# Optimization experiments

Measured on AMD Instinct MI355X. Metric: run time of the kernel, lower is better.

The kernel has to match this reference:

```python
import jax, jax.numpy as jnp
import numpy as np

N_OUT, N_CONS, N_AGE = 7, 20, 15
H = 256
B, T = 64, 365
D_ECO = N_CONS + N_AGE          # 35: eco+age feed the shared eco LSTM
D_BR = 1 + 3 + H                # 260: init + 3 age cols + eco LSTM output


def setup_inputs() -> dict:
    key = jax.random.key(0)
    ks = jax.random.split(key, 24)
    s = 0.05
    w = lambda k, shape: (jax.random.normal(k, shape, jnp.float32) * s)
    z = lambda shape: jnp.zeros(shape, jnp.float32)
    return {
        "inputs": jax.random.normal(ks[0], (B, T, N_CONS + N_OUT + N_AGE), jnp.float32),
        # shared eco LSTM (n_lstm_eco = 1)
        "eco_Wk": w(ks[1], (D_ECO, 4 * H)), "eco_Wr": w(ks[2], (H, 4 * H)), "eco_b": z((4 * H,)),
        # per-output data LSTMs (tanh)
        "data_Wk": w(ks[3], (N_OUT, D_BR, 4 * H)), "data_Wr": w(ks[4], (N_OUT, H, 4 * H)), "data_b": z((N_OUT, 4 * H)),
        # per-output attention LSTMs (activation='sigmoid')
        "att_Wk": w(ks[5], (N_OUT, D_BR, 4 * H)), "att_Wr": w(ks[6], (N_OUT, H, 4 * H)), "att_b": z((N_OUT, 4 * H)),
        # per-output tsOut LSTMs (return last state)
        "ts_Wk": w(ks[7], (N_OUT, H, 4 * H)), "ts_Wr": w(ks[8], (N_OUT, H, 4 * H)), "ts_b": z((N_OUT, 4 * H)),
        # per-output dense heads
        "d1_W": w(ks[9], (N_OUT, H, 256)), "d1_b": z((N_OUT, 256)),
        "d2_W": w(ks[10], (N_OUT, 256, 64)), "d2_b": z((N_OUT, 64)),
        "df_W": w(ks[11], (N_OUT, 64 + 3, 1)), "df_b": z((N_OUT, 1)),
    }


def _lstm(x, Wk, Wr, b, act):
    """Keras-style LSTM. x: [B,T,D]. Returns (all hidden [B,T,H], last hidden [B,H])."""
    Bc = x.shape[0]
    Hc = Wr.shape[0]
    xW = jnp.einsum('btd,dg->btg', x, Wk) + b      # precompute input projections

    def step(carry, xt):
        h, c = carry
        zi, zf, zg, zo = jnp.split(xt + h @ Wr, 4, axis=-1)  # Keras gate order i,f,c,o
        c = jax.nn.sigmoid(zf) * c + jax.nn.sigmoid(zi) * act(zg)
        h = jax.nn.sigmoid(zo) * act(c)
        return (h, c), h

    init = (jnp.zeros((Bc, Hc), x.dtype), jnp.zeros((Bc, Hc), x.dtype))
    (hT, _), hs = jax.lax.scan(step, init, jnp.swapaxes(xW, 0, 1))
    return jnp.swapaxes(hs, 0, 1), hT


def _branch(init_i, age_i, dWk, dWr, db, aWk, aWr, ab, tWk, tWr, tb, w1, b1, w2, b2, wf, bf, x_ecos):
    # init_i: [B,T,1], age_i: [B,T,3], x_ecos: [B,T,H] (shared)
    cur_input = jnp.concatenate([init_i, age_i, x_ecos], axis=-1)  # [B,T,260]
    data_hs, _ = _lstm(cur_input, dWk, dWr, db, jnp.tanh)
    att_hs, _ = _lstm(cur_input, aWk, aWr, ab, jax.nn.sigmoid)     # activation='sigmoid'
    _, h_last = _lstm(data_hs * att_hs, tWk, tWr, tb, jnp.tanh)    # return_sequences=False
    h = jax.nn.relu(h_last @ w1 + b1)
    h = jax.nn.relu(h @ w2 + b2)
    h = jnp.concatenate([h, cur_input[:, -1, 1:4]], axis=-1)       # append last-step age cols
    out = h @ wf + bf + cur_input[:, -1, :1]                       # residual add of last init
    return out  # [B,1]


def reference(inputs, eco_Wk, eco_Wr, eco_b, data_Wk, data_Wr, data_b,
              att_Wk, att_Wr, att_b, ts_Wk, ts_Wr, ts_b,
              d1_W, d1_b, d2_W, d2_b, df_W, df_b):
    x_init = inputs[:, :, N_CONS:N_CONS + N_OUT]                       # [B,T,7]
    x_age = inputs[:, :, N_CONS + N_OUT:N_CONS + N_OUT + N_AGE]        # [B,T,15]
    x_eco = inputs[:, :, :N_CONS]                                      # [B,T,20]

    x_ecos, _ = _lstm(jnp.concatenate([x_eco, x_age], axis=-1), eco_Wk, eco_Wr, eco_b, jnp.tanh)  # [B,T,256]

    init_i = jnp.moveaxis(x_init, 2, 0)[..., None]                     # [7,B,T,1]
    i_idx = jnp.arange(N_OUT)
    age_cols = jnp.stack([jnp.zeros_like(i_idx), i_idx + 1, i_idx + 8], axis=1)  # [7,3]
    age_i = jnp.moveaxis(x_age[:, :, age_cols], 2, 0)                  # [7,B,T,3]

    outs = jax.vmap(_branch, in_axes=(0,) * 17 + (None,))(
        init_i, age_i, data_Wk, data_Wr, data_b, att_Wk, att_Wr, att_b,
        ts_Wk, ts_Wr, ts_b, d1_W, d1_b, d2_W, d2_b, df_W, df_b, x_ecos)  # [7,B,1]
    return jnp.transpose(outs[:, :, 0])  # [B,7]
```

## Files before the change

### kernel.cpp

```cpp
#include <hip/hip_runtime.h>


#define TT 365
#define RE 4
#define RS 4

typedef short bf16x8 __attribute__((ext_vector_type(8)));
typedef float f32x4 __attribute__((ext_vector_type(4)));

__device__ __forceinline__ float b2f(unsigned short u) {
  union { unsigned u32; float f; } v; v.u32 = ((unsigned)u) << 16; return v.f;
}
__device__ __forceinline__ unsigned short f2b(float f) {
  union { float f; unsigned u32; } v; v.f = f;
  unsigned u = v.u32;
  u = u + 0x7FFFu + ((u >> 16) & 1u);
  return (unsigned short)(u >> 16);
}
__device__ __forceinline__ float sigf(float x) { return 1.0f / (1.0f + __expf(-x)); }
__device__ __forceinline__ float tanh_(float x) { return 2.0f / (1.0f + __expf(-2.0f * x)) - 1.0f; }

__device__ __forceinline__ unsigned long long ld64(const unsigned long long* p) {
  return __hip_atomic_load(p, __ATOMIC_RELAXED, __HIP_MEMORY_SCOPE_AGENT);
}
__device__ __forceinline__ void st64(unsigned long long* p, unsigned long long v) {
  __hip_atomic_store(p, v, __ATOMIC_RELAXED, __HIP_MEMORY_SCOPE_AGENT);
}
__device__ __forceinline__ unsigned ld32(const unsigned* p) {
  return __hip_atomic_load(p, __ATOMIC_RELAXED, __HIP_MEMORY_SCOPE_AGENT);
}
__device__ __forceinline__ void st32(unsigned* p, unsigned v) {
  __hip_atomic_store(p, v, __ATOMIC_RELAXED, __HIP_MEMORY_SCOPE_AGENT);
}
__device__ __forceinline__ unsigned long long tag2(unsigned tag, float a, float b) {
  return ((unsigned long long)tag << 32) | (unsigned)f2b(a) | ((unsigned)f2b(b) << 16);
}

__global__ __launch_bounds__(256) void k0a_wr(const float* __restrict__ eco_Wr,
    const float* __restrict__ data_Wr, const float* __restrict__ att_Wr,
    const float* __restrict__ ts_Wr, unsigned short* __restrict__ wr_swz)
{
  __shared__ float ls[32 * 133];
  const int kb = blockIdx.x, wg = blockIdx.y, l = blockIdx.z, tid = threadIdx.x;
  const float* src;
  if (l == 0) src = eco_Wr;
  else if (l < 15) { int d = l - 1; src = ((d & 1) ? att_Wr : data_Wr) + (size_t)(d >> 1) * 262144; }
  else src = ts_Wr + (size_t)(l - 15) * 262144;
  for (int e = tid; e < 4096; e += 256) {
    int ks = e >> 7, col = e & 127;
    int gate = col >> 5, hi = col & 31;
    ls[ks * 133 + col] = src[(size_t)(kb * 32 + ks) * 1024 + gate * 256 + wg * 32 + hi];
  }
  __syncthreads();
  unsigned short* out = wr_swz + (((size_t)l * 8 + wg) * 8 + kb) * 4096;
  for (int e = tid; e < 4096; e += 256) {
    int col = e >> 5, ks = e & 31;
    out[e] = f2b(ls[ks * 133 + col]);
  }
}

__global__ __launch_bounds__(256) void k0b_wk(const float* __restrict__ data_Wk,
    const float* __restrict__ att_Wk, const float* __restrict__ ts_Wk,
    unsigned short* __restrict__ wk_da, unsigned short* __restrict__ wk_ts)
{
  __shared__ float ls[32 * 261];
  const int cc = blockIdx.x, kb = blockIdx.y, d = blockIdx.z, tid = threadIdx.x;
  const float* src; unsigned short* dst; int roff;
  if (d < 14) { src = ((d & 1) ? att_Wk : data_Wk) + (size_t)(d >> 1) * 266240;
                dst = wk_da + (size_t)d * 262144; roff = 4; }
  else { src = ts_Wk + (size_t)(d - 14) * 262144;
         dst = wk_ts + (size_t)(d - 14) * 262144; roff = 0; }
  for (int e = tid; e < 8192; e += 256) {
    int ks = e >> 8, c2 = e & 255;
    ls[ks * 261 + c2] = src[(size_t)(roff + kb * 32 + ks) * 1024 + cc * 256 + c2];
  }
  __syncthreads();
  for (int e = tid; e < 8192; e += 256) {
    int col2 = e >> 5, ks = e & 31;
    dst[(size_t)kb * 32768 + (cc * 256 + col2) * 32 + ks] = f2b(ls[ks * 261 + col2]);
  }
}

__global__ __launch_bounds__(256) void k1_ecoxw(const float* __restrict__ inputs,
    const float* __restrict__ eco_Wk, const float* __restrict__ eco_b,
    unsigned short* __restrict__ xw_eco)
{
  __shared__ float Asl[64 * 35];
  __shared__ float Bsl[35 * 256];
  const int tg = blockIdx.x, ct = blockIdx.y, tid = threadIdx.x;
  for (int i = tid; i < 64 * 35; i += 256) {
    int b = i / 35, k = i - b * 35;
    int col = (k < 20) ? k : (k + 7);
    Asl[i] = inputs[((size_t)b * TT + tg) * 42 + col];
  }
  for (int i = tid; i < 35 * 256; i += 256) {
    int k = i >> 8, c = i & 255;
    Bsl[i] = eco_Wk[(size_t)k * 1024 + ct * 256 + c];
  }
  __syncthreads();
  const float bias = eco_b[ct * 256 + tid];
  for (int r = 0; r < 64; ++r) {
    float s = bias;
    #pragma unroll
    for (int k = 0; k < 35; ++k) s += Asl[r * 35 + k] * Bsl[k * 256 + tid];
    xw_eco[((size_t)tg * 64 + r) * 1024 + ct * 256 + tid] = f2b(s);
  }
}

__global__ __launch_bounds__(256, 1) void kP(
    const unsigned short* __restrict__ wr_swz,
    const unsigned short* __restrict__ wk_da,
    const unsigned short* __restrict__ wk_ts,
    const unsigned short* __restrict__ xw_eco,
    const float* __restrict__ inputs,
    const float* __restrict__ data_Wk, const float* __restrict__ att_Wk,
    const float* __restrict__ data_b, const float* __restrict__ att_b,
    const float* __restrict__ ts_b,
    unsigned long long* __restrict__ hE,
    unsigned long long* __restrict__ hD,
    unsigned long long* __restrict__ hsD,
    unsigned long long* __restrict__ hsA,
    unsigned long long* __restrict__ h2,
    unsigned* __restrict__ hDf, unsigned* __restrict__ h2f,
    unsigned* __restrict__ roleCtr,
    float* __restrict__ h_last)
{
  __shared__ __align__(16) unsigned char smem[160256];
  __shared__ int role_s;
  const int tid = threadIdx.x;
  if (tid == 0) {
    unsigned xcc;
    asm volatile("s_getreg_b32 %0, hwreg(HW_REG_XCC_ID)" : "=s"(xcc));
    xcc &= 7u;
    unsigned slot = atomicAdd(&roleCtr[xcc], 1u);
    role_s = (int)(xcc * 256u + slot);
  }
  __syncthreads();
  const int xcd = role_s >> 8, slot = role_s & 255;
  if (slot >= 32) return;
  const int lane = tid & 63, w = tid >> 6, c = lane & 15, grp = lane >> 4;

  if (xcd == 7) {
    if (slot >= 16) return;
    unsigned short* WR = (unsigned short*)smem;
    unsigned short* Hs = (unsigned short*)(smem + 81920);
    float* zsh = (float*)(smem + 102400);
    float* cst = (float*)(smem + 119296);
    const int wg = slot >> 1, bg = slot & 1;
    const unsigned short* wr_g = wr_swz + (size_t)wg * 32768;
    for (int i = tid * 8; i < 32768; i += 2048) {
      int kb = i >> 12; int rr = i & 4095; int col = rr >> 5; int ks = rr & 31;
      *(uint4*)&WR[(kb * 128 + col) * 40 + ks] = *(const uint4*)&wr_g[i];
    }
    for (int i = tid; i < 1024; i += 256) cst[i] = 0.0f;

    int xoff[16];
    #pragma unroll
    for (int rt = 0; rt < 2; ++rt)
      #pragma unroll
      for (int ct = 0; ct < 2; ++ct)
        #pragma unroll
        for (int rg = 0; rg < 4; ++rg)
          xoff[(rt * 2 + ct) * 4 + rg] =
              (bg * 32 + rt * 16 + grp * 4 + rg) * 1024 + w * 256 + wg * 32 + ct * 16 + c;
    unsigned short xv[16], xn[16];
    #pragma unroll
    for (int i = 0; i < 16; ++i) xv[i] = xw_eco[xoff[i]];
    __syncthreads();

    for (int t = 0; t < TT; ++t) {
      if (t + 1 > RE && tid < 112) {
        while ((int)ld32(&hDf[tid]) < t + 1 - RE) __builtin_amdgcn_s_sleep(2);
      }
      {
        const unsigned long long* hb = hE + (size_t)(t % RE) * 8192;
        unsigned long long v[16];
        #pragma unroll
        for (int i = 0; i < 16; ++i) {
          int m = tid + i * 256;
          v[i] = ld64(&hb[(bg * 32 + (m >> 7)) * 128 + (m & 127)]);
        }
        const unsigned tagv = (unsigned)t;
        int tries = 0;
        while (true) {
          unsigned pend = 0u;
          #pragma unroll
          for (int i = 0; i < 16; ++i)
            pend |= ((unsigned)(v[i] >> 32) != tagv) ? (1u << i) : 0u;
          if (!pend) break;
          if (++tries > 8) __builtin_amdgcn_s_sleep(1);
          #pragma unroll
          for (int i = 0; i < 16; ++i)
            if (pend & (1u << i)) {
              int m = tid + i * 256;
              v[i] = ld64(&hb[(bg * 32 + (m >> 7)) * 128 + (m & 127)]);
            }
        }
        #pragma unroll
        for (int i = 0; i < 16; ++i) {
          int m = tid + i * 256, row = m >> 7, kp = m & 127;
          *(unsigned int*)&Hs[((kp >> 4) * 32 + row) * 40 + 2 * (kp & 15)] = (unsigned int)v[i];
        }
      }
      __syncthreads();
      f32x4 acc[4];
      #pragma unroll
      for (int i = 0; i < 4; ++i)
        #pragma unroll
        for (int rg = 0; rg < 4; ++rg) acc[i][rg] = b2f(xv[i * 4 + rg]);
      if (t + 1 < TT) {
        const unsigned short* xw1 = xw_eco + (size_t)(t + 1) * 65536;
        #pragma unroll
        for (int i = 0; i < 16; ++i) xn[i] = xw1[xoff[i]];
      }
      #pragma unroll
      for (int kb = 0; kb < 8; ++kb) {
        bf16x8 a0 = *(const bf16x8*)&Hs[(kb * 32 + c) * 40 + grp * 8];
        bf16x8 a1 = *(const bf16x8*)&Hs[(kb * 32 + 16 + c) * 40 + grp * 8];
        bf16x8 b0 = *(const bf16x8*)&WR[(kb * 128 + w * 32 + c) * 40 + grp * 8];
        bf16x8 b1 = *(const bf16x8*)&WR[(kb * 128 + w * 32 + 16 + c) * 40 + grp * 8];
        acc[0] = __builtin_amdgcn_mfma_f32_16x16x32_bf16(a0, b0, acc[0], 0, 0, 0);
        acc[1] = __builtin_amdgcn_mfma_f32_16x16x32_bf16(a0, b1, acc[1], 0, 0, 0);
        acc[2] = __builtin_amdgcn_mfma_f32_16x16x32_bf16(a1, b0, acc[2], 0, 0, 0);
        acc[3] = __builtin_amdgcn_mfma_f32_16x16x32_bf16(a1, b1, acc[3], 0, 0, 0);
      }
      #pragma unroll
      for (int i = 0; i < 4; ++i) {
        int rt = i >> 1, ct = i & 1;
        #pragma unroll
        for (int rg = 0; rg < 4; ++rg)
          zsh[(rt * 16 + grp * 4 + rg) * 132 + w * 32 + ct * 16 + c] = acc[i][rg];
      }
      __syncthreads();
      {
        int row = tid >> 3, hq8 = tid & 7;
        float4 zi = *(const float4*)&zsh[row * 132 +      hq8 * 4];
        float4 zf = *(const float4*)&zsh[row * 132 + 32 + hq8 * 4];
        float4 zg = *(const float4*)&zsh[row * 132 + 64 + hq8 * 4];
        float4 zo = *(const float4*)&zsh[row * 132 + 96 + hq8 * 4];
        float4 c0 = *(const float4*)&cst[row * 32 + hq8 * 4];
        float cn0 = sigf(zf.x) * c0.x + sigf(zi.x) * tanh_(zg.x);
        float cn1 = sigf(zf.y) * c0.y + sigf(zi.y) * tanh_(zg.y);
        float cn2 = sigf(zf.z) * c0.z + sigf(zi.z) * tanh_(zg.z);
        float cn3 = sigf(zf.w) * c0.w + sigf(zi.w) * tanh_(zg.w);
        float hv0 = sigf(zo.x) * tanh_(cn0);
        float hv1 = sigf(zo.y) * tanh_(cn1);
        float hv2 = sigf(zo.z) * tanh_(cn2);
        float hv3 = sigf(zo.w) * tanh_(cn3);
        *(float4*)&cst[row * 32 + hq8 * 4] = make_float4(cn0, cn1, cn2, cn3);
        unsigned long long* ho = hE + (size_t)((t + 1) % RE) * 8192
                               + (bg * 32 + row) * 128 + wg * 16 + hq8 * 2;
        st64(&ho[0], tag2(t + 1, hv0, hv1));
        st64(&ho[1], tag2(t + 1, hv2, hv3));
      }
      #pragma unroll
      for (int i = 0; i < 16; ++i) xv[i] = xn[i];
    }
  } else if (slot < 16) {
    unsigned short* WR = (unsigned short*)smem;
    unsigned short* Hs = (unsigned short*)(smem + 81920);
    float* zsh = (float*)(smem + 122880);
    float* a_sp = (float*)(smem + 156672);
    float* b_sp = (float*)(smem + 157696);
    float* bias_s = (float*)(smem + 159744);
    const int l1 = xcd * 2 + (slot >> 3), colwg = slot & 7, br = xcd;
    const int q = l1 * 8 + colwg;
    const bool act_sig = (l1 & 1);
    const unsigned short* wr_g = wr_swz + ((size_t)(1 + l1) * 8 + colwg) * 32768;
    for (int i = tid * 8; i < 32768; i += 2048) {
      int kb = i >> 12; int rr = i & 4095; int col = rr >> 5; int ks = rr & 31;
      *(uint4*)&WR[(kb * 128 + col) * 40 + ks] = *(const uint4*)&wr_g[i];
    }
    bf16x8 wkf[16];
    const unsigned short* wk = wk_da + (size_t)l1 * 262144;
    #pragma unroll
    for (int kb = 0; kb < 8; ++kb)
      #pragma unroll
      for (int ct = 0; ct < 2; ++ct) {
        int col = w * 256 + colwg * 32 + ct * 16 + c;
        wkf[kb * 2 + ct] = *(const bf16x8*)&wk[kb * 32768 + col * 32 + grp * 8];
      }
    const float* spWk = (act_sig ? att_Wk : data_Wk) + (size_t)br * 266240;
    for (int i = tid; i < 512; i += 256) {
      int j = i >> 7, colL = i & 127;
      int gcol = (colL >> 5) * 256 + colwg * 32 + (colL & 31);
      b_sp[i] = spWk[(size_t)j * 1024 + gcol];
    }
    if (tid < 128) {
      int gcol = (tid >> 5) * 256 + colwg * 32 + (tid & 31);
      bias_s[tid] = (act_sig ? att_b : data_b)[br * 1024 + gcol];
    }
    float creg[8];
    #pragma unroll
    for (int j = 0; j < 8; ++j) creg[j] = 0.0f;
    unsigned long long* hDl = hD + (size_t)l1 * 2 * 8192;
    unsigned long long* ring = (act_sig ? hsA : hsD) + (size_t)br * RS * 8192;
    __syncthreads();

    for (int t = 0; t < TT; ++t) {
      if (t + 1 > RS && tid < 16) {
        while ((int)ld32(&h2f[br * 16 + tid]) < t + 1 - RS) __builtin_amdgcn_s_sleep(2);
      }
      if (tid < 64) {
        const float* ip = inputs + ((size_t)tid * TT + t) * 42;
        a_sp[tid * 4 + 0] = ip[20 + br];
        a_sp[tid * 4 + 1] = ip[27];
        a_sp[tid * 4 + 2] = ip[27 + br + 1];
        a_sp[tid * 4 + 3] = ip[27 + br + 8];
      }
      const unsigned long long* he = hE + (size_t)((t + 1) % RE) * 8192;
      const unsigned long long* ho = hDl + (size_t)(t & 1) * 8192;
      unsigned long long ve[32], vh[32];
      #pragma unroll
      for (int i = 0; i < 32; ++i) ve[i] = ld64(&he[tid + i * 256]);
      #pragma unroll
      for (int i = 0; i < 32; ++i) vh[i] = ld64(&ho[tid + i * 256]);
      {
        const unsigned tagv = (unsigned)(t + 1);
        int tries = 0;
        while (true) {
          unsigned long long pend = 0ull;
          #pragma unroll
          for (int i = 0; i < 32; ++i)
            pend |= ((unsigned)(ve[i] >> 32) != tagv) ? (1ull << i) : 0ull;
          if (!pend) break;
          if (++tries > 8) __builtin_amdgcn_s_sleep(1);
          #pragma unroll
          for (int i = 0; i < 32; ++i)
            if (pend & (1ull << i)) ve[i] = ld64(&he[tid + i * 256]);
        }
      }
      #pragma unroll
      for (int i = 0; i < 32; ++i) {
        int m = tid + i * 256, row = m >> 7, kp = m & 127;
        *(unsigned int*)&Hs[((kp >> 4) * 64 + row) * 40 + 2 * (kp & 15)] = (unsigned int)ve[i];
      }
      __syncthreads();
      if (tid == 0) st32(&hDf[q], (unsigned)(t + 1));
      f32x4 acc[8] = {};
      #pragma unroll
      for (int kb = 0; kb < 8; ++kb) {
        bf16x8 a[4];
        #pragma unroll
        for (int rt = 0; rt < 4; ++rt)
          a[rt] = *(const bf16x8*)&Hs[(kb * 64 + rt * 16 + c) * 40 + grp * 8];
        #pragma unroll
        for (int rt = 0; rt < 4; ++rt)
          #pragma unroll
          for (int ct = 0; ct < 2; ++ct)
            acc[rt * 2 + ct] = __builtin_amdgcn_mfma_f32_16x16x32_bf16(a[rt], wkf[kb * 2 + ct], acc[rt * 2 + ct], 0, 0, 0);
      }
      #pragma unroll
      for (int i = 0; i < 8; ++i) {
        int rt = i >> 1, ct2 = i & 1;
        #pragma unroll
        for (int rg = 0; rg < 4; ++rg) {
          int row = rt * 16 + grp * 4 + rg;
          int colL = w * 32 + ct2 * 16 + c;
          acc[i][rg] += bias_s[colL]
                      + a_sp[row * 4 + 0] * b_sp[colL]       + a_sp[row * 4 + 1] * b_sp[128 + colL]
                      + a_sp[row * 4 + 2] * b_sp[256 + colL] + a_sp[row * 4 + 3] * b_sp[384 + colL];
        }
      }
      {
        const unsigned tagv = (unsigned)t;
        int tries = 0;
        while (true) {
          unsigned long long pend = 0ull;
          #pragma unroll
          for (int i = 0; i < 32; ++i)
            pend |= ((unsigned)(vh[i] >> 32) != tagv) ? (1ull << i) : 0ull;
          if (!pend) break;
          if (++tries > 8) __builtin_amdgcn_s_sleep(1);
          #pragma unroll
          for (int i = 0; i < 32; ++i)
            if (pend & (1ull << i)) vh[i] = ld64(&ho[tid + i * 256]);
        }
      }
      __syncthreads();
      #pragma unroll
      for (int i = 0; i < 32; ++i) {
        int m = tid + i * 256, row = m >> 7, kp = m & 127;
        *(unsigned int*)&Hs[((kp >> 4) * 64 + row) * 40 + 2 * (kp & 15)] = (unsigned int)vh[i];
      }
      __syncthreads();
      #pragma unroll
      for (int kb = 0; kb < 8; ++kb) {
        bf16x8 a[4]; bf16x8 b[2];
        #pragma unroll
        for (int rt = 0; rt < 4; ++rt)
          a[rt] = *(const bf16x8*)&Hs[(kb * 64 + rt * 16 + c) * 40 + grp * 8];
        #pragma unroll
        for (int ct = 0; ct < 2; ++ct)
          b[ct] = *(const bf16x8*)&WR[(kb * 128 + w * 32 + ct * 16 + c) * 40 + grp * 8];
        #pragma unroll
        for (int rt = 0; rt < 4; ++rt)
          #pragma unroll
          for (int ct = 0; ct < 2; ++ct)
            acc[rt * 2 + ct] = __builtin_amdgcn_mfma_f32_16x16x32_bf16(a[rt], b[ct], acc[rt * 2 + ct], 0, 0, 0);
      }
      #pragma unroll
      for (int i = 0; i < 8; ++i) {
        int rt = i >> 1, ct2 = i & 1;
        #pragma unroll
        for (int rg = 0; rg < 4; ++rg)
          zsh[(rt * 16 + grp * 4 + rg) * 132 + w * 32 + ct2 * 16 + c] = acc[i][rg];
      }
      __syncthreads();
      {
        unsigned long long* hon = hDl + (size_t)((t + 1) & 1) * 8192;
        unsigned long long* rs = ring + (size_t)(t % RS) * 8192;
        #pragma unroll
        for (int it = 0; it < 2; ++it) {
          int m = tid + it * 256, row = m >> 3, hq8 = m & 7;
          float4 zi = *(const float4*)&zsh[row * 132 +      hq8 * 4];
          float4 zf = *(const float4*)&zsh[row * 132 + 32 + hq8 * 4];
          float4 zg = *(const float4*)&zsh[row * 132 + 64 + hq8 * 4];
          float4 zo = *(const float4*)&zsh[row * 132 + 96 + hq8 * 4];
          float g0 = act_sig ? sigf(zg.x) : tanh_(zg.x);
          float g1 = act_sig ? sigf(zg.y) : tanh_(zg.y);
          float g2 = act_sig ? sigf(zg.z) : tanh_(zg.z);
          float g3 = act_sig ? sigf(zg.w) : tanh_(zg.w);
          float cn0 = sigf(zf.x) * creg[it * 4 + 0] + sigf(zi.x) * g0;
          float cn1 = sigf(zf.y) * creg[it * 4 + 1] + sigf(zi.y) * g1;
          float cn2 = sigf(zf.z) * creg[it * 4 + 2] + sigf(zi.z) * g2;
          float cn3 = sigf(zf.w) * creg[it * 4 + 3] + sigf(zi.w) * g3;
          float hv0 = sigf(zo.x) * (act_sig ? sigf(cn0) : tanh_(cn0));
          float hv1 = sigf(zo.y) * (act_sig ? sigf(cn1) : tanh_(cn1));
          float hv2 = sigf(zo.z) * (act_sig ? sigf(cn2) : tanh_(cn2));
          float hv3 = sigf(zo.w) * (act_sig ? sigf(cn3) : tanh_(cn3));
          creg[it * 4 + 0] = cn0; creg[it * 4 + 1] = cn1;
          creg[it * 4 + 2] = cn2; creg[it * 4 + 3] = cn3;
          int kp = colwg * 16 + hq8 * 2;
          unsigned long long w0 = tag2(t + 1, hv0, hv1);
          unsigned long long w1 = tag2(t + 1, hv2, hv3);
          st64(&hon[row * 128 + kp], w0);
          st64(&hon[row * 128 + kp + 1], w1);
          st64(&rs[row * 128 + kp], w0);
          st64(&rs[row * 128 + kp + 1], w1);
        }
      }
    }
  } else {
    unsigned short* WR = (unsigned short*)smem;
    unsigned short* Hs = (unsigned short*)(smem + 81920);
    float* zsh = (float*)(smem + 102400);
    float* bias_s = (float*)(smem + 119296);
    const int d = xcd, sub = slot - 16, colwg = sub >> 1, bg = sub & 1;
    const unsigned short* wr_g = wr_swz + ((size_t)(15 + d) * 8 + colwg) * 32768;
    for (int i = tid * 8; i < 32768; i += 2048) {
      int kb = i >> 12; int rr = i & 4095; int col = rr >> 5; int ks = rr & 31;
      *(uint4*)&WR[(kb * 128 + col) * 40 + ks] = *(const uint4*)&wr_g[i];
    }
    bf16x8 wkf[16];
    const unsigned short* wk = wk_ts + (size_t)d * 262144;
    #pragma unroll
    for (int kb = 0; kb < 8; ++kb)
      #pragma unroll
      for (int ct = 0; ct < 2; ++ct) {
        int col = w * 256 + colwg * 32 + ct * 16 + c;
        wkf[kb * 2 + ct] = *(const bf16x8*)&wk[kb * 32768 + col * 32 + grp * 8];
      }
    if (tid < 128) {
      int gcol = (tid >> 5) * 256 + colwg * 32 + (tid & 31);
      bias_s[tid] = ts_b[d * 1024 + gcol];
    }
    float creg[4] = {0.0f, 0.0f, 0.0f, 0.0f};
    const unsigned long long* rD = hsD + (size_t)d * RS * 8192;
    const unsigned long long* rA = hsA + (size_t)d * RS * 8192;
    unsigned long long* h2d = h2 + (size_t)d * 2 * 8192;
    __syncthreads();

    for (int t = 0; t < TT; ++t) {
      const unsigned long long* sd = rD + (size_t)(t % RS) * 8192;
      const unsigned long long* sa = rA + (size_t)(t % RS) * 8192;
      const unsigned long long* ho = h2d + (size_t)(t & 1) * 8192;
      unsigned long long vd[16], va[16], vh[16];
      int idx16[16];
      #pragma unroll
      for (int i = 0; i < 16; ++i) {
        int m = tid + i * 256;
        idx16[i] = (bg * 32 + (m >> 7)) * 128 + (m & 127);
      }
      #pragma unroll
      for (int i = 0; i < 16; ++i) vd[i] = ld64(&sd[idx16[i]]);
      #pragma unroll
      for (int i = 0; i < 16; ++i) va[i] = ld64(&sa[idx16[i]]);
      #pragma unroll
      for (int i = 0; i < 16; ++i) vh[i] = ld64(&ho[idx16[i]]);
      {
        const unsigned tagv = (unsigned)(t + 1);
        int tries = 0;
        while (true) {
          unsigned pend = 0u;
          #pragma unroll
          for (int i = 0; i < 16; ++i) {
            pend |= ((unsigned)(vd[i] >> 32) != tagv) ? (1u << i) : 0u;
            pend |= ((unsigned)(va[i] >> 32) != tagv) ? (0x10000u << i) : 0u;
          }
          if (!pend) break;
          if (++tries > 8) __builtin_amdgcn_s_sleep(1);
          #pragma unroll
          for (int i = 0; i < 16; ++i) {
            if (pend & (1u << i)) vd[i] = ld64(&sd[idx16[i]]);
            if (pend & (0x10000u << i)) va[i] = ld64(&sa[idx16[i]]);
          }
        }
      }
      #pragma unroll
      for (int i = 0; i < 16; ++i) {
        int m = tid + i * 256, row = m >> 7, kp = m & 127;
        unsigned dl = (unsigned)vd[i], al = (unsigned)va[i];
        float p0 = b2f((unsigned short)dl) * b2f((unsigned short)al);
        float p1 = b2f((unsigned short)(dl >> 16)) * b2f((unsigned short)(al >> 16));
        unsigned pv = (unsigned)f2b(p0) | ((unsigned)f2b(p1) << 16);
        *(unsigned int*)&Hs[((kp >> 4) * 32 + row) * 40 + 2 * (kp & 15)] = pv;
      }
      __syncthreads();
      if (tid == 0) st32(&h2f[d * 16 + sub], (unsigned)(t + 1));
      f32x4 acc[4] = {};
      #pragma unroll
      for (int kb = 0; kb < 8; ++kb) {
        bf16x8 a0 = *(const bf16x8*)&Hs[(kb * 32 + c) * 40 + grp * 8];
        bf16x8 a1 = *(const bf16x8*)&Hs[(kb * 32 + 16 + c) * 40 + grp * 8];
        acc[0] = __builtin_amdgcn_mfma_f32_16x16x32_bf16(a0, wkf[kb * 2 + 0], acc[0], 0, 0, 0);
        acc[1] = __builtin_amdgcn_mfma_f32_16x16x32_bf16(a0, wkf[kb * 2 + 1], acc[1], 0, 0, 0);
        acc[2] = __builtin_amdgcn_mfma_f32_16x16x32_bf16(a1, wkf[kb * 2 + 0], acc[2], 0, 0, 0);
        acc[3] = __builtin_amdgcn_mfma_f32_16x16x32_bf16(a1, wkf[kb * 2 + 1], acc[3], 0, 0, 0);
      }
      #pragma unroll
      for (int i = 0; i < 4; ++i) {
        int ct2 = i & 1;
        #pragma unroll
        for (int rg = 0; rg < 4; ++rg)
          acc[i][rg] += bias_s[w * 32 + ct2 * 16 + c];
      }
      {
        const unsigned tagv = (unsigned)t;
        int tries = 0;
        while (true) {
          unsigned pend = 0u;
          #pragma unroll
          for (int i = 0; i < 16; ++i)
            pend |= ((unsigned)(vh[i] >> 32) != tagv) ? (1u << i) : 0u;
          if (!pend) break;
          if (++tries > 8) __builtin_amdgcn_s_sleep(1);
          #pragma unroll
          for (int i = 0; i < 16; ++i)
            if (pend & (1u << i)) vh[i] = ld64(&ho[idx16[i]]);
        }
      }
      __syncthreads();
      #pragma unroll
      for (int i = 0; i < 16; ++i) {
        int m = tid + i * 256, row = m >> 7, kp = m & 127;
        *(unsigned int*)&Hs[((kp >> 4) * 32 + row) * 40 + 2 * (kp & 15)] = (unsigned int)vh[i];
      }
      __syncthreads();
      #pragma unroll
      for (int kb = 0; kb < 8; ++kb) {
        bf16x8 a0 = *(const bf16x8*)&Hs[(kb * 32 + c) * 40 + grp * 8];
        bf16x8 a1 = *(const bf16x8*)&Hs[(kb * 32 + 16 + c) * 40 + grp * 8];
        bf16x8 b0 = *(const bf16x8*)&WR[(kb * 128 + w * 32 + c) * 40 + grp * 8];
        bf16x8 b1 = *(const bf16x8*)&WR[(kb * 128 + w * 32 + 16 + c) * 40 + grp * 8];
        acc[0] = __builtin_amdgcn_mfma_f32_16x16x32_bf16(a0, b0, acc[0], 0, 0, 0);
        acc[1] = __builtin_amdgcn_mfma_f32_16x16x32_bf16(a0, b1, acc[1], 0, 0, 0);
        acc[2] = __builtin_amdgcn_mfma_f32_16x16x32_bf16(a1, b0, acc[2], 0, 0, 0);
        acc[3] = __builtin_amdgcn_mfma_f32_16x16x32_bf16(a1, b1, acc[3], 0, 0, 0);
      }
      #pragma unroll
      for (int i = 0; i < 4; ++i) {
        int rt = i >> 1, ct2 = i & 1;
        #pragma unroll
        for (int rg = 0; rg < 4; ++rg)
          zsh[(rt * 16 + grp * 4 + rg) * 132 + w * 32 + ct2 * 16 + c] = acc[i][rg];
      }
      __syncthreads();
      {
        int row = tid >> 3, hq8 = tid & 7;
        float4 zi = *(const float4*)&zsh[row * 132 +      hq8 * 4];
        float4 zf = *(const float4*)&zsh[row * 132 + 32 + hq8 * 4];
        float4 zg = *(const float4*)&zsh[row * 132 + 64 + hq8 * 4];
        float4 zo = *(const float4*)&zsh[row * 132 + 96 + hq8 * 4];
        float cn0 = sigf(zf.x) * creg[0] + sigf(zi.x) * tanh_(zg.x);
        float cn1 = sigf(zf.y) * creg[1] + sigf(zi.y) * tanh_(zg.y);
        float cn2 = sigf(zf.z) * creg[2] + sigf(zi.z) * tanh_(zg.z);
        float cn3 = sigf(zf.w) * creg[3] + sigf(zi.w) * tanh_(zg.w);
        float hv0 = sigf(zo.x) * tanh_(cn0);
        float hv1 = sigf(zo.y) * tanh_(cn1);
        float hv2 = sigf(zo.z) * tanh_(cn2);
        float hv3 = sigf(zo.w) * tanh_(cn3);
        creg[0] = cn0; creg[1] = cn1; creg[2] = cn2; creg[3] = cn3;
        unsigned long long* hn = h2d + (size_t)((t + 1) & 1) * 8192
                               + (bg * 32 + row) * 128 + colwg * 16 + hq8 * 2;
        st64(&hn[0], tag2(t + 1, hv0, hv1));
        st64(&hn[1], tag2(t + 1, hv2, hv3));
        if (t == TT - 1) {
          *(float4*)&h_last[(size_t)d * 16384 + (bg * 32 + row) * 256 + colwg * 32 + hq8 * 4]
              = make_float4(hv0, hv1, hv2, hv3);
        }
      }
    }
  }
}

__global__ __launch_bounds__(256) void k7_d1(const float* __restrict__ h_last,
    const float* __restrict__ d1_W, const float* __restrict__ d1_b, float* __restrict__ d1o)
{
  __shared__ float Asl[64 * 256];
  __shared__ float Bsl[256 * 64];
  const int nt = blockIdx.x, br = blockIdx.y, tid = threadIdx.x;
  const float* hl = h_last + (size_t)br * 16384;
  for (int i = tid; i < 16384; i += 256) Asl[i] = hl[i];
  const float* wp = d1_W + (size_t)br * 65536 + nt * 64;
  for (int i = tid; i < 16384; i += 256) {
    int k = i >> 6, cl = i & 63;
    Bsl[i] = wp[(size_t)k * 256 + cl];
  }
  __syncthreads();
  const int cl = tid & 63, rq = tid >> 6;
  float s[16];
  const float bias = d1_b[br * 256 + nt * 64 + cl];
  #pragma unroll
  for (int i = 0; i < 16; ++i) s[i] = bias;
  for (int k = 0; k < 256; ++k) {
    float bv = Bsl[k * 64 + cl];
    #pragma unroll
    for (int i = 0; i < 16; ++i) s[i] += Asl[(rq * 16 + i) * 256 + k] * bv;
  }
  #pragma unroll
  for (int i = 0; i < 16; ++i)
    d1o[(size_t)br * 16384 + (rq * 16 + i) * 256 + nt * 64 + cl] = fmaxf(s[i], 0.0f);
}

__global__ __launch_bounds__(256) void k8_head(const float* __restrict__ d1o,
    const float* __restrict__ d2_W, const float* __restrict__ d2_b,
    const float* __restrict__ df_W, const float* __restrict__ df_b,
    const float* __restrict__ inputs, float* __restrict__ out)
{
  __shared__ float Asl[64 * 256];
  __shared__ float Bsl[256 * 64];
  __shared__ float d2sT[64 * 65];
  __shared__ float wfs[68];
  const int br = blockIdx.x, tid = threadIdx.x;
  for (int i = tid; i < 16384; i += 256) Asl[i] = d1o[(size_t)br * 16384 + i];
  for (int i = tid; i < 16384; i += 256) Bsl[i] = d2_W[(size_t)br * 16384 + i];
  if (tid < 67) wfs[tid] = df_W[br * 67 + tid];
  __syncthreads();
  const int cl = tid & 63, rq = tid >> 6;
  float s[16];
  const float bias = d2_b[br * 64 + cl];
  #pragma unroll
  for (int i = 0; i < 16; ++i) s[i] = bias;
  for (int k = 0; k < 256; ++k) {
    float bv = Bsl[k * 64 + cl];
    #pragma unroll
    for (int i = 0; i < 16; ++i) s[i] += Asl[(rq * 16 + i) * 256 + k] * bv;
  }
  #pragma unroll
  for (int i = 0; i < 16; ++i) d2sT[cl * 65 + rq * 16 + i] = fmaxf(s[i], 0.0f);
  __syncthreads();
  if (tid < 64) {
    const int b = tid;
    const float* ip = inputs + ((size_t)b * TT + (TT - 1)) * 42;
    float acc = df_b[br] + ip[20 + br] + ip[27] * wfs[64] + ip[27 + br + 1] * wfs[65]
              + ip[27 + br + 8] * wfs[66];
    #pragma unroll 4
    for (int j = 0; j < 64; ++j) acc += d2sT[j * 65 + b] * wfs[j];
    out[b * 7 + br] = acc;
  }
}

extern "C" void kernel_launch(void* const* d_in, const int* in_sizes, int n_in,
                              void* d_out, int out_size, void* d_ws, size_t ws_size,
                              hipStream_t stream) {
  (void)in_sizes; (void)n_in; (void)out_size;
  const float* inputs  = (const float*)d_in[0];
  const float* eco_Wk  = (const float*)d_in[1];
  const float* eco_Wr  = (const float*)d_in[2];
  const float* eco_b   = (const float*)d_in[3];
  const float* data_Wk = (const float*)d_in[4];
  const float* data_Wr = (const float*)d_in[5];
  const float* data_b  = (const float*)d_in[6];
  const float* att_Wk  = (const float*)d_in[7];
  const float* att_Wr  = (const float*)d_in[8];
  const float* att_b   = (const float*)d_in[9];
  const float* ts_Wk   = (const float*)d_in[10];
  const float* ts_Wr   = (const float*)d_in[11];
  const float* ts_b    = (const float*)d_in[12];
  const float* d1_W    = (const float*)d_in[13];
  const float* d1_b    = (const float*)d_in[14];
  const float* d2_W    = (const float*)d_in[15];
  const float* d2_b    = (const float*)d_in[16];
  const float* df_W    = (const float*)d_in[17];
  const float* df_b    = (const float*)d_in[18];

  char* ws = (char*)d_ws;
  size_t off = 0;
  auto take = [&](size_t bytes) -> void* {
    void* p = ws + off;
    off += (bytes + 255) & ~(size_t)255;
    return p;
  };
  unsigned short* wr_swz = (unsigned short*)take((size_t)22 * 262144 * 2);
  unsigned short* wk_da  = (unsigned short*)take((size_t)14 * 262144 * 2);
  unsigned short* wk_ts  = (unsigned short*)take((size_t)7  * 262144 * 2);
  unsigned short* xw_eco = (unsigned short*)take((size_t)TT * 65536 * 2);
  float*          h_last = (float*)take((size_t)7 * 16384 * 4);
  float*          d1o    = (float*)take((size_t)7 * 16384 * 4);
  size_t sync_begin = off;
  unsigned long long* hE  = (unsigned long long*)take((size_t)RE * 8192 * 8);
  unsigned long long* hD  = (unsigned long long*)take((size_t)14 * 2 * 8192 * 8);
  unsigned long long* hsD = (unsigned long long*)take((size_t)7 * RS * 8192 * 8);
  unsigned long long* hsA = (unsigned long long*)take((size_t)7 * RS * 8192 * 8);
  unsigned long long* h2  = (unsigned long long*)take((size_t)7 * 2 * 8192 * 8);
  unsigned* hDf = (unsigned*)take(112 * 4);
  unsigned* h2f = (unsigned*)take(112 * 4);
  unsigned* roleCtr = (unsigned*)take(16 * 4);
  size_t sync_bytes = off - sync_begin;
  if (off > ws_size) return;

  hipMemsetAsync(ws + sync_begin, 0, sync_bytes, stream);
  k0a_wr<<<dim3(8, 8, 22), 256, 0, stream>>>(eco_Wr, data_Wr, att_Wr, ts_Wr, wr_swz);
  k0b_wk<<<dim3(4, 8, 21), 256, 0, stream>>>(data_Wk, att_Wk, ts_Wk, wk_da, wk_ts);
  k1_ecoxw<<<dim3(TT, 4), 256, 0, stream>>>(inputs, eco_Wk, eco_b, xw_eco);
  kP<<<256, 256, 0, stream>>>(wr_swz, wk_da, wk_ts, xw_eco, inputs,
                              data_Wk, att_Wk, data_b, att_b, ts_b,
                              hE, hD, hsD, hsA, h2, hDf, h2f, roleCtr, h_last);
  k7_d1<<<dim3(4, 7), 256, 0, stream>>>(h_last, d1_W, d1_b, d1o);
  k8_head<<<7, 256, 0, stream>>>(d1o, d2_W, d2_b, df_W, df_b, inputs, (float*)d_out);
}
```

Measured before the change: 4.077 ms.

## Add per-workgroup progress flags so consumers poll a few counters before reading tagged data

Each producer workgroup now publishes a per-step progress counter after a block barrier, and consumers spin on a handful of these 64-bit flag words before loading the tagged hidden-state rings. The aim is to cut the cost of repeatedly polling many tagged data words across the whole grid, replacing it with cheap flag polling. It adds an extra __syncthreads per step in every role and a flag-store, which may lengthen the per-step critical path. The existing tag checks are kept, so the flags only add another layer of waiting.

```diff
diff --git a/kernel.cpp b/kernel.cpp
--- a/kernel.cpp
+++ b/kernel.cpp
@@ -32,8 +32,24 @@
 __device__ __forceinline__ void st32(unsigned* p, unsigned v) {
   __hip_atomic_store(p, v, __ATOMIC_RELAXED, __HIP_MEMORY_SCOPE_AGENT);
 }
+__device__ __forceinline__ unsigned umin_(unsigned a, unsigned b) { return a < b ? a : b; }
 __device__ __forceinline__ unsigned long long tag2(unsigned tag, float a, float b) {
   return ((unsigned long long)tag << 32) | (unsigned)f2b(a) | ((unsigned)f2b(b) << 16);
+}
+template<int NP>
+__device__ __forceinline__ void flag_wait(const unsigned* flags, unsigned tv) {
+  const unsigned long long* fp = (const unsigned long long*)flags;
+  int tries = 0;
+  while (true) {
+    unsigned mn = 0xffffffffu;
+    #pragma unroll
+    for (int i = 0; i < NP; ++i) {
+      unsigned long long v = ld64(&fp[i]);
+      mn = umin_(mn, umin_((unsigned)v, (unsigned)(v >> 32)));
+    }
+    if (mn >= tv) break;
+    if (++tries > 12) __builtin_amdgcn_s_sleep(2);
+  }
 }
 
 __global__ __launch_bounds__(256) void k0a_wr(const float* __restrict__ eco_Wr,
@@ -122,6 +138,8 @@
     unsigned long long* __restrict__ hsA,
     unsigned long long* __restrict__ h2,
     unsigned* __restrict__ hDf, unsigned* __restrict__ h2f,
+    unsigned* __restrict__ fE, unsigned* __restrict__ f1,
+    unsigned* __restrict__ f2,
     unsigned* __restrict__ roleCtr,
     float* __restrict__ h_last)
 {
@@ -172,6 +190,7 @@
       if (t + 1 > RE && tid < 112) {
         while ((int)ld32(&hDf[tid]) < t + 1 - RE) __builtin_amdgcn_s_sleep(2);
       }
+      flag_wait<8>(fE, (unsigned)t);
       {
         const unsigned long long* hb = hE + (size_t)(t % RE) * 8192;
         unsigned long long v[16];
@@ -253,6 +272,8 @@
         st64(&ho[0], tag2(t + 1, hv0, hv1));
         st64(&ho[1], tag2(t + 1, hv2, hv3));
       }
+      __syncthreads();
+      if (tid == 0) st32(&fE[slot], (unsigned)(t + 1));
       #pragma unroll
       for (int i = 0; i < 16; ++i) xv[i] = xn[i];
     }
@@ -308,6 +329,7 @@
         a_sp[tid * 4 + 2] = ip[27 + br + 1];
         a_sp[tid * 4 + 3] = ip[27 + br + 8];
       }
+      flag_wait<8>(fE, (unsigned)(t + 1));
       const unsigned long long* he = hE + (size_t)((t + 1) % RE) * 8192;
       const unsigned long long* ho = hDl + (size_t)(t & 1) * 8192;
       unsigned long long ve[32], vh[32];
@@ -362,6 +384,7 @@
                       + a_sp[row * 4 + 2] * b_sp[256 + colL] + a_sp[row * 4 + 3] * b_sp[384 + colL];
         }
       }
+      flag_wait<4>(f1 + l1 * 8, (unsigned)t);
       {
         const unsigned tagv = (unsigned)t;
         int tries = 0;
@@ -440,6 +463,8 @@
           st64(&rs[row * 128 + kp + 1], w1);
         }
       }
+      __syncthreads();
+      if (tid == 0) st32(&f1[q], (unsigned)(t + 1));
     }
   } else {
     unsigned short* WR = (unsigned short*)smem;
@@ -472,6 +497,27 @@
     __syncthreads();
 
     for (int t = 0; t < TT; ++t) {
+      {
+        const unsigned long long* fp1 = (const unsigned long long*)(f1 + d * 16);
+        const unsigned long long* fp2 = (const unsigned long long*)(f2 + d * 16);
+        const unsigned tv1 = (unsigned)(t + 1), tv2 = (unsigned)t;
+        int tries = 0;
+        while (true) {
+          unsigned mn1 = 0xffffffffu, mn2 = 0xffffffffu;
+          #pragma unroll
+          for (int i = 0; i < 8; ++i) {
+            unsigned long long v = ld64(&fp1[i]);
+            mn1 = umin_(mn1, umin_((unsigned)v, (unsigned)(v >> 32)));
+          }
+          #pragma unroll
+          for (int i = 0; i < 8; ++i) {
+            unsigned long long v = ld64(&fp2[i]);
+            mn2 = umin_(mn2, umin_((unsigned)v, (unsigned)(v >> 32)));
+          }
+          if (mn1 >= tv1 && mn2 >= tv2) break;
+          if (++tries > 12) __builtin_amdgcn_s_sleep(2);
+        }
+      }
       const unsigned long long* sd = rD + (size_t)(t % RS) * 8192;
       const unsigned long long* sa = rA + (size_t)(t % RS) * 8192;
       const unsigned long long* ho = h2d + (size_t)(t & 1) * 8192;
@@ -600,6 +646,8 @@
               = make_float4(hv0, hv1, hv2, hv3);
         }
       }
+      __syncthreads();
+      if (tid == 0) st32(&f2[d * 16 + sub], (unsigned)(t + 1));
     }
   }
 }
@@ -716,6 +764,9 @@
   unsigned long long* h2  = (unsigned long long*)take((size_t)7 * 2 * 8192 * 8);
   unsigned* hDf = (unsigned*)take(112 * 4);
   unsigned* h2f = (unsigned*)take(112 * 4);
+  unsigned* fE  = (unsigned*)take(16 * 4);
+  unsigned* f1  = (unsigned*)take(112 * 4);
+  unsigned* f2  = (unsigned*)take(112 * 4);
   unsigned* roleCtr = (unsigned*)take(16 * 4);
   size_t sync_bytes = off - sync_begin;
   if (off > ws_size) return;
@@ -726,7 +777,8 @@
   k1_ecoxw<<<dim3(TT, 4), 256, 0, stream>>>(inputs, eco_Wk, eco_b, xw_eco);
   kP<<<256, 256, 0, stream>>>(wr_swz, wk_da, wk_ts, xw_eco, inputs,
                               data_Wk, att_Wk, data_b, att_b, ts_b,
-                              hE, hD, hsD, hsA, h2, hDf, h2f, roleCtr, h_last);
+                              hE, hD, hsD, hsA, h2, hDf, h2f, fE, f1, f2,
+                              roleCtr, h_last);
   k7_d1<<<dim3(4, 7), 256, 0, stream>>>(h_last, d1_W, d1_b, d1o);
   k8_head<<<7, 256, 0, stream>>>(d1o, d2_W, d2_b, df_W, df_b, inputs, (float*)d_out);
 }
```

New measurement: 4.473 ms. 1.1x slower.
